# Performance work log

Measured on AMD Instinct MI355X. Metric: run time of the kernel, lower is better.

The kernel has to match this reference:

```python
import jax, jax.numpy as jnp
import numpy as np

# Geometry constants (mirror the torch module's config)
HO = 512          # output height (self.ho)
WO = 512          # output width  (self.wo)
TILE = 128        # tile_sz (= h of each MPI tile)
PAD = 8           # tile_pad_sz (config.render_padsz)
HP = TILE + 2 * PAD          # padded tile side = 144
P = HP * HP                  # pixels per warped plane = 20736
BH = HO + TILE + 2 * PAD     # buffer height = 656
BW = WO + TILE + 2 * PAD     # buffer width  = 656
HW = BH * BW
B = 1
S = 512                      # nt * n planes


def setup_inputs() -> dict:
    key = jax.random.key(0)
    k0, k1, k2, k3, k4 = jax.random.split(key, 5)
    tgt_rgb = jax.random.uniform(k0, (B, S, 3, P), dtype=jnp.float32)
    tgt_sigma = jax.random.uniform(k1, (B, S, P), dtype=jnp.float32)
    mpi_depth = jax.random.uniform(k2, (B, S), dtype=jnp.float32) * 10.0 + 0.1
    sx = jax.random.randint(k3, (B, S), 0, HO - TILE + 1, dtype=jnp.int32)
    sy = jax.random.randint(k4, (B, S), 0, WO - TILE + 1, dtype=jnp.int32)
    return {"tgt_rgb": tgt_rgb, "tgt_sigma": tgt_sigma, "mpi_depth": mpi_depth,
            "sx": sx, "sy": sy}


def reference(tgt_rgb, tgt_sigma, mpi_depth, sx, sy):
    b = tgt_rgb.shape[0]
    # --- depth sort (front-to-back), mirroring torch.sort + fancy gather ---
    order = jnp.argsort(mpi_depth, axis=1)                                  # [b,S]
    depth_s = jnp.take_along_axis(mpi_depth, order, axis=1)                 # [b,S]
    sx_s = jnp.take_along_axis(sx, order, axis=1)
    sy_s = jnp.take_along_axis(sy, order, axis=1)
    rgb_s = jnp.take_along_axis(tgt_rgb, order[:, :, None, None], axis=1)   # [b,S,3,P]
    sig_s = jnp.take_along_axis(tgt_sigma, order[:, :, None], axis=1)       # [b,S,P]

    yy, xx = jnp.meshgrid(jnp.arange(HP, dtype=jnp.int32),
                          jnp.arange(HP, dtype=jnp.int32), indexing='ij')
    yy = yy.reshape(-1)  # [P]
    xx = xx.reshape(-1)  # [P]
    bi = jnp.arange(b)[:, None]            # [b,1]
    ci = jnp.arange(3)[None, :, None]      # [1,3,1]

    def plane_step(carry, inp):
        trans, out_rgb, out_depth = carry          # [b,HW], [b,3,HW], [b,HW]
        rgb, sig, dep, px, py = inp                # [b,3,P],[b,P],[b],[b],[b]
        idx = (yy[None, :] + py[:, None]) * BW + (xx[None, :] + px[:, None])  # [b,P]
        tg = jnp.take_along_axis(trans, idx, axis=1)                          # gather T
        w = sig * tg                                                          # alpha*T
        out_rgb = out_rgb.at[bi[:, :, None], ci, idx[:, None, :]].add(rgb * w[:, None, :])
        out_depth = out_depth.at[bi, idx].add(dep[:, None] * w)
        trans = trans.at[bi, idx].set(tg * (1.0 - sig))
        return (trans, out_rgb, out_depth), None

    carry0 = (jnp.ones((b, HW), jnp.float32),
              jnp.zeros((b, 3, HW), jnp.float32),
              jnp.zeros((b, HW), jnp.float32))
    xs = (rgb_s.transpose(1, 0, 2, 3), sig_s.transpose(1, 0, 2),
          depth_s.T, sx_s.T, sy_s.T)
    (trans, out_rgb, out_depth), _ = jax.lax.scan(plane_step, carry0, xs)

    img = out_rgb.reshape(b, 3, BH, BW)
    # crop: [PAD : BH-TILE-PAD, PAD : BW-TILE-PAD] -> [b,3,HO,WO]
    img = img[:, :, PAD:BH - TILE - PAD, PAD:BW - TILE - PAD]
    return img
```

## Files before the change

kernel.cpp:

```cpp
#include <hip/hip_runtime.h>

constexpr int TILE   = 128;
constexpr int PAD    = 8;
constexpr int HP     = TILE + 2 * PAD;
constexpr int P      = HP * HP;
constexpr int S      = 512;
constexpr int OUTW   = 512;
constexpr int OUTP   = OUTW * OUTW;
constexpr int NSEG   = 8;
constexpr int NCHUNK = OUTW / 64;
constexpr int BAND   = 8;
constexpr int CAP    = 128;
constexpr int GROUP  = 8;
constexpr float TEPS = 1e-3f;

__global__ __launch_bounds__(512) void sort_planes_kernel(
    const float* __restrict__ depth,
    const int*   __restrict__ sx,
    const int*   __restrict__ sy,
    int4*        __restrict__ meta)
{
    __shared__ float sd[S];
    const int i = threadIdx.x;
    sd[i] = depth[i];
    __syncthreads();

    const float di = sd[i];
    int rank = 0;
#pragma unroll 8
    for (int j = 0; j < S; ++j) {
        const float dj = sd[j];
        rank += (dj < di) || (dj == di && j < i);
    }
    meta[rank] = make_int4(sy[i], sx[i], i * P, i * 3 * P);
}

__global__ __launch_bounds__(512) void fused_composite_kernel(
    const float* __restrict__ rgb,
    const float* __restrict__ sigma,
    const int4*  __restrict__ meta,
    float*       __restrict__ out)
{
    __shared__ int4 slist[CAP];
    __shared__ int  cnt[NSEG];

    const int tid  = threadIdx.x;
    const int w    = tid >> 6;
    const int lane = tid & 63;
    const int X0   = blockIdx.x * 64;
    const int Y0   = blockIdx.y * BAND;

    const int4 m = meta[tid];
    const bool cov =
        ((unsigned)(Y0 + PAD + BAND - 1 - m.x) < (unsigned)(HP + BAND - 1)) &&
        ((unsigned)(X0 + 71 - m.y) < 207u);
    const unsigned long long mask = __ballot(cov);
    const int pre = __popcll(mask & ((1ull << lane) - 1ull));
    if (lane == 0) cnt[w] = __popcll(mask);
    __syncthreads();

    int off = 0, nc = 0;
#pragma unroll
    for (int i = 0; i < NSEG; ++i) {
        const int c = cnt[i];
        off += (i < w) ? c : 0;
        nc  += c;
    }
    const int padded = min((nc + GROUP - 1) & ~(GROUP - 1), CAP);
    if (cov) {
        const int idx = off + pre;
        if (idx < CAP) slist[idx] = m;
    }
    if (tid >= nc && tid < padded) slist[tid] = make_int4(-100000, -100000, 0, 0);
    __syncthreads();

    const int row = Y0 + w;
    const int yb  = row + PAD;
    const int xb  = X0 + PAD + lane;

    float trans = 1.0f, ar = 0.0f, ag = 0.0f, ab = 0.0f;
    for (int k = 0; k < padded; k += GROUP) {
#pragma unroll
        for (int u = 0; u < GROUP; ++u) {
            const int4 e = slist[k + u];
            const int yy = yb - e.x;
            const int xx = xb - e.y;
            const bool c = ((unsigned)yy < (unsigned)HP) &
                           ((unsigned)xx < (unsigned)HP);
            const int  yc = min(max(yy, 0), HP - 1);
            const int  xc = min(max(xx, 0), HP - 1);
            const int  o  = yc * HP + xc;
            float sg = sigma[e.z + o];
            sg = c ? sg : 0.0f;
            const int   pr  = e.w + o;
            const float wgt = sg * trans;
            ar = fmaf(rgb[pr],         wgt, ar);
            ag = fmaf(rgb[pr + P],     wgt, ag);
            ab = fmaf(rgb[pr + 2 * P], wgt, ab);
            trans *= (1.0f - sg);
        }
        if (__all(trans < TEPS)) break;
    }

    const int o = row * OUTW + X0 + lane;
    out[o]            = ar;
    out[o + OUTP]     = ag;
    out[o + 2 * OUTP] = ab;
}

extern "C" void kernel_launch(void* const* d_in, const int* in_sizes, int n_in,
                              void* d_out, int out_size, void* d_ws, size_t ws_size,
                              hipStream_t stream)
{
    const float* tgt_rgb   = (const float*)d_in[0];
    const float* tgt_sigma = (const float*)d_in[1];
    const float* mpi_depth = (const float*)d_in[2];
    const int*   sx        = (const int*)d_in[3];
    const int*   sy        = (const int*)d_in[4];
    float*       out       = (float*)d_out;
    int4*        meta      = (int4*)d_ws;

    sort_planes_kernel<<<1, S, 0, stream>>>(mpi_depth, sx, sy, meta);

    dim3 grid(NCHUNK, OUTW / BAND);
    fused_composite_kernel<<<grid, 512, 0, stream>>>(tgt_rgb, tgt_sigma,
                                                     meta, out);
}
```

Measured before the change: 39.88 us.

## Process two columns per thread with batched loads and reshaped block tile

Each block now covers 4 rows by 128 columns with 256 threads, and each thread composites two pixels 64 columns apart. Per group of 8 planes, all sigma and rgb loads are issued up front into register arrays before the serial transmittance update, so more memory requests are in flight at once. The plane-list build runs in two halves over 512 planes, and the list capacity grows to 192 because the wider tile overlaps more planes. The cost is higher register pressure, a longer per-block plane list, and the early exit now waiting until both pixels are saturated.

```diff
diff --git a/kernel.cpp b/kernel.cpp
--- a/kernel.cpp
+++ b/kernel.cpp
@@ -7,10 +7,10 @@
 constexpr int S      = 512;
 constexpr int OUTW   = 512;
 constexpr int OUTP   = OUTW * OUTW;
-constexpr int NSEG   = 8;
-constexpr int NCHUNK = OUTW / 64;
-constexpr int BAND   = 8;
-constexpr int CAP    = 128;
+constexpr int BAND   = 4;
+constexpr int WCOLS  = 128;
+constexpr int NWAVE  = 4;
+constexpr int CAP    = 192;
 constexpr int GROUP  = 8;
 constexpr float TEPS = 1e-3f;
 
@@ -35,77 +35,110 @@
     meta[rank] = make_int4(sy[i], sx[i], i * P, i * 3 * P);
 }
 
-__global__ __launch_bounds__(512) void fused_composite_kernel(
+__global__ __launch_bounds__(256) void fused_composite_kernel(
     const float* __restrict__ rgb,
     const float* __restrict__ sigma,
     const int4*  __restrict__ meta,
     float*       __restrict__ out)
 {
     __shared__ int4 slist[CAP];
-    __shared__ int  cnt[NSEG];
+    __shared__ int  cnt[2][NWAVE];
 
     const int tid  = threadIdx.x;
     const int w    = tid >> 6;
     const int lane = tid & 63;
-    const int X0   = blockIdx.x * 64;
+    const int X0   = blockIdx.x * WCOLS;
     const int Y0   = blockIdx.y * BAND;
 
-    const int4 m = meta[tid];
-    const bool cov =
-        ((unsigned)(Y0 + PAD + BAND - 1 - m.x) < (unsigned)(HP + BAND - 1)) &&
-        ((unsigned)(X0 + 71 - m.y) < 207u);
-    const unsigned long long mask = __ballot(cov);
-    const int pre = __popcll(mask & ((1ull << lane) - 1ull));
-    if (lane == 0) cnt[w] = __popcll(mask);
-    __syncthreads();
+    int total = 0;
+#pragma unroll
+    for (int h = 0; h < 2; ++h) {
+        const int4 m = meta[h * 256 + tid];
+        const bool cov =
+            ((unsigned)(Y0 + PAD + BAND - 1 - m.x) < (unsigned)(HP + BAND - 1)) &&
+            ((unsigned)(X0 + PAD + WCOLS - 1 - m.y) < (unsigned)(HP + WCOLS - 1));
+        const unsigned long long bm = __ballot(cov);
+        const int pre = __popcll(bm & ((1ull << lane) - 1ull));
+        if (lane == 0) cnt[h][w] = __popcll(bm);
+        __syncthreads();
 
-    int off = 0, nc = 0;
+        int off = 0, hs = 0;
 #pragma unroll
-    for (int i = 0; i < NSEG; ++i) {
-        const int c = cnt[i];
-        off += (i < w) ? c : 0;
-        nc  += c;
+        for (int i = 0; i < NWAVE; ++i) {
+            const int c = cnt[h][i];
+            off += (i < w) ? c : 0;
+            hs  += c;
+        }
+        if (cov) {
+            const int idx = total + off + pre;
+            if (idx < CAP) slist[idx] = m;
+        }
+        total += hs;
     }
-    const int padded = min((nc + GROUP - 1) & ~(GROUP - 1), CAP);
-    if (cov) {
-        const int idx = off + pre;
-        if (idx < CAP) slist[idx] = m;
-    }
-    if (tid >= nc && tid < padded) slist[tid] = make_int4(-100000, -100000, 0, 0);
+    const int padded = min((total + GROUP - 1) & ~(GROUP - 1), CAP);
+    if (tid >= total && tid < padded) slist[tid] = make_int4(-100000, -100000, 0, 0);
     __syncthreads();
 
     const int row = Y0 + w;
     const int yb  = row + PAD;
-    const int xb  = X0 + PAD + lane;
+    const int x0  = X0 + PAD + lane;
+    const int x1  = x0 + 64;
 
-    float trans = 1.0f, ar = 0.0f, ag = 0.0f, ab = 0.0f;
+    float t0 = 1.0f, a0r = 0.0f, a0g = 0.0f, a0b = 0.0f;
+    float t1 = 1.0f, a1r = 0.0f, a1g = 0.0f, a1b = 0.0f;
+
     for (int k = 0; k < padded; k += GROUP) {
+        float s0[GROUP], m0[GROUP], r0[GROUP], g0[GROUP], b0[GROUP];
+        float s1[GROUP], m1[GROUP], r1[GROUP], g1[GROUP], b1[GROUP];
 #pragma unroll
         for (int u = 0; u < GROUP; ++u) {
             const int4 e = slist[k + u];
-            const int yy = yb - e.x;
-            const int xx = xb - e.y;
-            const bool c = ((unsigned)yy < (unsigned)HP) &
-                           ((unsigned)xx < (unsigned)HP);
-            const int  yc = min(max(yy, 0), HP - 1);
-            const int  xc = min(max(xx, 0), HP - 1);
-            const int  o  = yc * HP + xc;
-            float sg = sigma[e.z + o];
-            sg = c ? sg : 0.0f;
-            const int   pr  = e.w + o;
-            const float wgt = sg * trans;
-            ar = fmaf(rgb[pr],         wgt, ar);
-            ag = fmaf(rgb[pr + P],     wgt, ag);
-            ab = fmaf(rgb[pr + 2 * P], wgt, ab);
-            trans *= (1.0f - sg);
+            const int yy  = yb - e.x;
+            const bool cy = (unsigned)yy < (unsigned)HP;
+            const int yc  = min(max(yy, 0), HP - 1);
+            const int xo0 = x0 - e.y;
+            const int xo1 = x1 - e.y;
+            const bool c0 = cy & ((unsigned)xo0 < (unsigned)HP);
+            const bool c1 = cy & ((unsigned)xo1 < (unsigned)HP);
+            const int xc0 = min(max(xo0, 0), HP - 1);
+            const int xc1 = min(max(xo1, 0), HP - 1);
+            const int o0  = yc * HP + xc0;
+            const int o1  = yc * HP + xc1;
+            m0[u] = c0 ? 1.0f : 0.0f;
+            m1[u] = c1 ? 1.0f : 0.0f;
+            s0[u] = sigma[e.z + o0];
+            s1[u] = sigma[e.z + o1];
+            const int p0 = e.w + o0;
+            const int p1 = e.w + o1;
+            r0[u] = rgb[p0];          r1[u] = rgb[p1];
+            g0[u] = rgb[p0 + P];      g1[u] = rgb[p1 + P];
+            b0[u] = rgb[p0 + 2 * P];  b1[u] = rgb[p1 + 2 * P];
         }
-        if (__all(trans < TEPS)) break;
+#pragma unroll
+        for (int u = 0; u < GROUP; ++u) {
+            const float sg0 = s0[u] * m0[u];
+            const float w0  = sg0 * t0;
+            a0r = fmaf(r0[u], w0, a0r);
+            a0g = fmaf(g0[u], w0, a0g);
+            a0b = fmaf(b0[u], w0, a0b);
+            t0 *= (1.0f - sg0);
+            const float sg1 = s1[u] * m1[u];
+            const float w1  = sg1 * t1;
+            a1r = fmaf(r1[u], w1, a1r);
+            a1g = fmaf(g1[u], w1, a1g);
+            a1b = fmaf(b1[u], w1, a1b);
+            t1 *= (1.0f - sg1);
+        }
+        if (__all((t0 < TEPS) & (t1 < TEPS))) break;
     }
 
     const int o = row * OUTW + X0 + lane;
-    out[o]            = ar;
-    out[o + OUTP]     = ag;
-    out[o + 2 * OUTP] = ab;
+    out[o]                 = a0r;
+    out[o + OUTP]          = a0g;
+    out[o + 2 * OUTP]      = a0b;
+    out[o + 64]            = a1r;
+    out[o + 64 + OUTP]     = a1g;
+    out[o + 64 + 2 * OUTP] = a1b;
 }
 
 extern "C" void kernel_launch(void* const* d_in, const int* in_sizes, int n_in,
@@ -122,7 +155,7 @@
 
     sort_planes_kernel<<<1, S, 0, stream>>>(mpi_depth, sx, sy, meta);
 
-    dim3 grid(NCHUNK, OUTW / BAND);
-    fused_composite_kernel<<<grid, 512, 0, stream>>>(tgt_rgb, tgt_sigma,
+    dim3 grid(OUTW / WCOLS, OUTW / BAND);
+    fused_composite_kernel<<<grid, 256, 0, stream>>>(tgt_rgb, tgt_sigma,
                                                      meta, out);
 }
```

Result: slower. 47.32 us (+18.7%).

## Batch plane loads per group, add block-wide early exit, loosen transmittance cutoff

Applied to the files above, without the earlier changes.

The composite loop now issues all sigma and RGB loads for a group of eight planes before doing the serial transmittance math, so more memory requests are in flight at once. Waves that finish no longer leave the loop on their own. They record a per-wave done flag in shared memory, and the whole block exits together after two barriers per group. The transmittance cutoff is raised from 1e-3 to 4e-3, which stops compositing earlier at the cost of a small accuracy loss that may be near the tolerance. The barriers also add synchronization cost and hold finished waves in the block.

```diff
diff --git a/kernel.cpp b/kernel.cpp
--- a/kernel.cpp
+++ b/kernel.cpp
@@ -12,7 +12,7 @@
 constexpr int BAND   = 8;
 constexpr int CAP    = 128;
 constexpr int GROUP  = 8;
-constexpr float TEPS = 1e-3f;
+constexpr float TEPS = 4e-3f;
 
 __global__ __launch_bounds__(512) void sort_planes_kernel(
     const float* __restrict__ depth,
@@ -43,6 +43,7 @@
 {
     __shared__ int4 slist[CAP];
     __shared__ int  cnt[NSEG];
+    __shared__ int  sdone[NSEG];
 
     const int tid  = threadIdx.x;
     const int w    = tid >> 6;
@@ -54,9 +55,9 @@
     const bool cov =
         ((unsigned)(Y0 + PAD + BAND - 1 - m.x) < (unsigned)(HP + BAND - 1)) &&
         ((unsigned)(X0 + 71 - m.y) < 207u);
-    const unsigned long long mask = __ballot(cov);
-    const int pre = __popcll(mask & ((1ull << lane) - 1ull));
-    if (lane == 0) cnt[w] = __popcll(mask);
+    const unsigned long long bmask = __ballot(cov);
+    const int pre = __popcll(bmask & ((1ull << lane) - 1ull));
+    if (lane == 0) cnt[w] = __popcll(bmask);
     __syncthreads();
 
     int off = 0, nc = 0;
@@ -79,27 +80,47 @@
     const int xb  = X0 + PAD + lane;
 
     float trans = 1.0f, ar = 0.0f, ag = 0.0f, ab = 0.0f;
+    bool wave_done = false;
+
     for (int k = 0; k < padded; k += GROUP) {
+        if (!wave_done) {
+            float s[GROUP], mk[GROUP], r[GROUP], g[GROUP], b[GROUP];
 #pragma unroll
-        for (int u = 0; u < GROUP; ++u) {
-            const int4 e = slist[k + u];
-            const int yy = yb - e.x;
-            const int xx = xb - e.y;
-            const bool c = ((unsigned)yy < (unsigned)HP) &
-                           ((unsigned)xx < (unsigned)HP);
-            const int  yc = min(max(yy, 0), HP - 1);
-            const int  xc = min(max(xx, 0), HP - 1);
-            const int  o  = yc * HP + xc;
-            float sg = sigma[e.z + o];
-            sg = c ? sg : 0.0f;
-            const int   pr  = e.w + o;
-            const float wgt = sg * trans;
-            ar = fmaf(rgb[pr],         wgt, ar);
-            ag = fmaf(rgb[pr + P],     wgt, ag);
-            ab = fmaf(rgb[pr + 2 * P], wgt, ab);
-            trans *= (1.0f - sg);
+            for (int u = 0; u < GROUP; ++u) {
+                const int4 e = slist[k + u];
+                const int yy = yb - e.x;
+                const int xx = xb - e.y;
+                const bool c = ((unsigned)yy < (unsigned)HP) &
+                               ((unsigned)xx < (unsigned)HP);
+                const int yc = min(max(yy, 0), HP - 1);
+                const int xc = min(max(xx, 0), HP - 1);
+                const int o  = yc * HP + xc;
+                mk[u] = c ? 1.0f : 0.0f;
+                s[u]  = sigma[e.z + o];
+                const int pr = e.w + o;
+                r[u] = rgb[pr];
+                g[u] = rgb[pr + P];
+                b[u] = rgb[pr + 2 * P];
+            }
+#pragma unroll
+            for (int u = 0; u < GROUP; ++u) {
+                const float sg  = s[u] * mk[u];
+                const float wgt = sg * trans;
+                ar = fmaf(r[u], wgt, ar);
+                ag = fmaf(g[u], wgt, ag);
+                ab = fmaf(b[u], wgt, ab);
+                trans *= (1.0f - sg);
+            }
+            wave_done = __all(trans < TEPS);
         }
-        if (__all(trans < TEPS)) break;
+        if (lane == 0) sdone[w] = wave_done ? 1 : 0;
+        asm volatile("s_waitcnt lgkmcnt(0)" ::: "memory");
+        __builtin_amdgcn_s_barrier();
+        const int alldone = sdone[0] & sdone[1] & sdone[2] & sdone[3] &
+                            sdone[4] & sdone[5] & sdone[6] & sdone[7];
+        asm volatile("s_waitcnt lgkmcnt(0)" ::: "memory");
+        __builtin_amdgcn_s_barrier();
+        if (alldone) break;
     }
 
     const int o = row * OUTW + X0 + lane;
```

Result: no change. 40.02 us (+0.4%).
